# Kernel optimization log

Hardware: AMD Instinct MI355X
Metric: run time of the kernel (lower is better)

Reference implementation:

```python
import jax, jax.numpy as jnp
import numpy as np

LN_EPS = 1e-5


def setup_inputs() -> dict:
    key = jax.random.key(0)
    ks = jax.random.split(key, 8)
    B, N, M, D = 4, 512, 512, 256
    s = 1.0 / np.sqrt(D)
    return {
        "x": jax.random.normal(ks[0], (B, N, D), jnp.float32),
        "c": jax.random.normal(ks[1], (B, M, D), jnp.float32),
        "mask": jnp.ones((B, N, M), jnp.float32),
        "Wq": jax.random.normal(ks[2], (D, D), jnp.float32) * s,
        "bq": jax.random.normal(ks[3], (D,), jnp.float32) * s,
        "Wk": jax.random.normal(ks[4], (D, D), jnp.float32) * s,
        "Wr": jax.random.normal(ks[5], (D,), jnp.float32) * s,
        "Wv": jax.random.normal(ks[6], (D, D), jnp.float32) * s,
        "bv": jax.random.normal(ks[7], (D,), jnp.float32) * s,
        "gamma": jnp.ones((D,), jnp.float32),
        "beta": jnp.zeros((D,), jnp.float32),
    }


def reference(x, c, mask, Wq, bq, Wk, Wr, Wv, bv, gamma, beta):
    D = x.shape[-1]
    deflator = 1.0 / jnp.sqrt(jnp.asarray(D, x.dtype))
    # q: (B, n, 1, d), k: (B, 1, m, d) -- Bahdanau-style additive scores
    q = jnp.tanh(jnp.einsum("bnd,ed->bne", x, Wq) + bq)[:, :, None, :]
    k = jnp.tanh(jnp.einsum("bmd,ed->bme", c, Wk))[:, None, :, :]
    # weight_reduce to scalar score, tanh then relu, squeeze last dim
    w = jax.nn.relu(jnp.tanh(jnp.einsum("bnmd,d->bnm", q + k, Wr)))
    w = w * mask
    v = (jnp.einsum("bmd,ed->bme", c, Wv) + bv) * deflator
    add = jnp.einsum("bnm,bmd->bnd", w, v)
    h = x + add
    mu = jnp.mean(h, axis=-1, keepdims=True)
    var = jnp.mean(jnp.square(h - mu), axis=-1, keepdims=True)
    return (h - mu) / jnp.sqrt(var + LN_EPS) * gamma + beta
```

## Files before the change

### kernel.cpp

```cpp
#include <hip/hip_runtime.h>
#include <math.h>

#define BB 4
#define NN 512
#define MM 512
#define DD 256

typedef short  s16x8  __attribute__((ext_vector_type(8)));
typedef __bf16 bf16x8 __attribute__((ext_vector_type(8)));
typedef __bf16 bf16x4 __attribute__((ext_vector_type(4)));
typedef float  f32x4  __attribute__((ext_vector_type(4)));
typedef float  f32x8  __attribute__((ext_vector_type(8)));
typedef unsigned short u16x4 __attribute__((ext_vector_type(4)));

static __device__ __forceinline__ f32x4 mfma16(s16x8 a, s16x8 b, f32x4 c) {
    return __builtin_amdgcn_mfma_f32_16x16x32_bf16(
        __builtin_bit_cast(bf16x8, a), __builtin_bit_cast(bf16x8, b), c, 0, 0, 0);
}

static __device__ __forceinline__ s16x8 cvt8(const float* __restrict__ p) {
    const float4 a = *(const float4*)p;
    const float4 b = *(const float4*)(p + 4);
    f32x8 f;
    f[0] = a.x; f[1] = a.y; f[2] = a.z; f[3] = a.w;
    f[4] = b.x; f[5] = b.y; f[6] = b.z; f[7] = b.w;
    return __builtin_bit_cast(s16x8, __builtin_convertvector(f, bf16x8));
}

static __device__ __forceinline__ u16x4 cvt4(float x, float y, float z, float w) {
    f32x4 f; f[0] = x; f[1] = y; f[2] = z; f[3] = w;
    return __builtin_bit_cast(u16x4, __builtin_convertvector(f, bf16x4));
}

static __device__ __forceinline__ float tanh_fast(float x) {
    const float e = __builtin_amdgcn_exp2f(x * 2.8853900817779268f);
    return fmaf(-2.0f, __builtin_amdgcn_rcpf(e + 1.0f), 1.0f);
}

__global__ __launch_bounds__(256) void k_proj(
    const float* __restrict__ x, const float* __restrict__ c,
    const float* __restrict__ Wq, const float* __restrict__ bq,
    const float* __restrict__ Wk, const float* __restrict__ Wr,
    const float* __restrict__ Wv, const float* __restrict__ bv,
    float* __restrict__ qs, float* __restrict__ ks,
    unsigned short* __restrict__ vT)
{
    __shared__ float red[4][16];
    const int tid  = threadIdx.x;
    const int lane = tid & 63, w = tid >> 6;
    const int li   = lane & 15, g = lane >> 4;
    const bool isk = blockIdx.x >= 128;
    const int row0 = (blockIdx.x & 127) << 4;
    const float* __restrict__ src = isk ? c : x;

    const float* ap = src + (size_t)(row0 + li) * DD + g * 8;
    s16x8 af[8];
    #pragma unroll
    for (int kk = 0; kk < 8; ++kk) af[kk] = cvt8(ap + kk * 32);

    const int e_base = w * 64 + li;

    if (!isk) {
        f32x4 acc[4];
        const float* bp[4];
        #pragma unroll
        for (int nt = 0; nt < 4; ++nt) {
            acc[nt] = (f32x4){0.f, 0.f, 0.f, 0.f};
            bp[nt] = Wq + (size_t)(e_base + nt * 16) * DD + g * 8;
        }
        #pragma unroll
        for (int kk = 0; kk < 8; ++kk)
            #pragma unroll
            for (int nt = 0; nt < 4; ++nt)
                acc[nt] = mfma16(af[kk], cvt8(bp[nt] + kk * 32), acc[nt]);

        float p[4] = {0.f, 0.f, 0.f, 0.f};
        #pragma unroll
        for (int nt = 0; nt < 4; ++nt) {
            const int e = e_base + nt * 16;
            const float bqe = bq[e], wre = Wr[e];
            #pragma unroll
            for (int r = 0; r < 4; ++r)
                p[r] += wre * tanh_fast(acc[nt][r] + bqe);
        }
        #pragma unroll
        for (int r = 0; r < 4; ++r) {
            p[r] += __shfl_xor(p[r], 1);
            p[r] += __shfl_xor(p[r], 2);
            p[r] += __shfl_xor(p[r], 4);
            p[r] += __shfl_xor(p[r], 8);
        }
        if (li == 0) {
            #pragma unroll
            for (int r = 0; r < 4; ++r) red[w][g * 4 + r] = p[r];
        }
        __syncthreads();
        if (tid < 16)
            qs[row0 + tid] = red[0][tid] + red[1][tid] + red[2][tid] + red[3][tid];
    } else {
        f32x4 ak[4], av[4];
        const float* bpk[4];
        const float* bpv[4];
        #pragma unroll
        for (int nt = 0; nt < 4; ++nt) {
            ak[nt] = (f32x4){0.f, 0.f, 0.f, 0.f};
            av[nt] = (f32x4){0.f, 0.f, 0.f, 0.f};
            bpk[nt] = Wk + (size_t)(e_base + nt * 16) * DD + g * 8;
            bpv[nt] = Wv + (size_t)(e_base + nt * 16) * DD + g * 8;
        }
        #pragma unroll
        for (int kk = 0; kk < 8; ++kk)
            #pragma unroll
            for (int nt = 0; nt < 4; ++nt) {
                ak[nt] = mfma16(af[kk], cvt8(bpk[nt] + kk * 32), ak[nt]);
                av[nt] = mfma16(af[kk], cvt8(bpv[nt] + kk * 32), av[nt]);
            }

        const int b  = row0 >> 9;
        const int m0 = row0 & 511;
        unsigned short* vTb = vT + (size_t)b * (DD * MM);
        #pragma unroll
        for (int nt = 0; nt < 4; ++nt) {
            const int e = e_base + nt * 16;
            const float bve = bv[e];
            const u16x4 o = cvt4((av[nt][0] + bve) * 0.0625f,
                                 (av[nt][1] + bve) * 0.0625f,
                                 (av[nt][2] + bve) * 0.0625f,
                                 (av[nt][3] + bve) * 0.0625f);
            *(u16x4*)(vTb + (size_t)e * MM + m0 + g * 4) = o;
        }

        float p[4] = {0.f, 0.f, 0.f, 0.f};
        #pragma unroll
        for (int nt = 0; nt < 4; ++nt) {
            const int e = e_base + nt * 16;
            const float wre = Wr[e];
            #pragma unroll
            for (int r = 0; r < 4; ++r)
                p[r] += wre * tanh_fast(ak[nt][r]);
        }
        #pragma unroll
        for (int r = 0; r < 4; ++r) {
            p[r] += __shfl_xor(p[r], 1);
            p[r] += __shfl_xor(p[r], 2);
            p[r] += __shfl_xor(p[r], 4);
            p[r] += __shfl_xor(p[r], 8);
        }
        if (li == 0) {
            #pragma unroll
            for (int r = 0; r < 4; ++r) red[w][g * 4 + r] = p[r];
        }
        __syncthreads();
        if (tid < 16)
            ks[row0 + tid] = red[0][tid] + red[1][tid] + red[2][tid] + red[3][tid];
    }
}

__global__ __launch_bounds__(256) void k_main(
    const float* __restrict__ x, const float* __restrict__ mask,
    const float* __restrict__ qs, const float* __restrict__ ks,
    const unsigned short* __restrict__ vT,
    const float* __restrict__ gamma, const float* __restrict__ beta,
    float* __restrict__ out)
{
    __shared__ unsigned short w_lds[16][512];
    __shared__ float ksm[MM];
    __shared__ float h_lds[16][264];
    const int tid  = threadIdx.x;
    const int lane = tid & 63, w = tid >> 6;
    const int li   = lane & 15, g = lane >> 4;
    const int n0g  = blockIdx.x << 3;
    const int b    = n0g >> 9;

    ksm[tid]       = ks[(b << 9) + tid];
    ksm[tid + 256] = ks[(b << 9) + 256 + tid];
    __syncthreads();

    char* wbase = (char*)w_lds;
    const float* __restrict__ mrow = mask + (size_t)n0g * MM;
    #pragma unroll
    for (int it = 0; it < 4; ++it) {
        const int L = (it << 10) + (tid << 2);
        const int i = L >> 9;
        const int m = L & 511;
        const float qv = qs[n0g + i];
        const float4 mk = *(const float4*)(mrow + (size_t)i * MM + m);
        const float4 kv = *(const float4*)&ksm[m];
        const u16x4 o = cvt4(fmaxf(tanh_fast(qv + kv.x), 0.f) * mk.x,
                             fmaxf(tanh_fast(qv + kv.y), 0.f) * mk.y,
                             fmaxf(tanh_fast(qv + kv.z), 0.f) * mk.z,
                             fmaxf(tanh_fast(qv + kv.w), 0.f) * mk.w);
        *(u16x4*)(wbase + (i << 10) + ((m << 1) ^ ((i & 7) << 4))) = o;
    }
    __syncthreads();

    f32x4 acc[4];
    const unsigned short* vp[4];
    #pragma unroll
    for (int nt = 0; nt < 4; ++nt) {
        acc[nt] = (f32x4){0.f, 0.f, 0.f, 0.f};
        vp[nt] = vT + (size_t)b * (DD * MM)
                    + (size_t)(w * 64 + nt * 16 + li) * MM + g * 8;
    }
    const char* arow = wbase + (li << 10);
    const int aswz = (li & 7) << 4;
    #pragma unroll
    for (int kk = 0; kk < 16; ++kk) {
        const s16x8 a = *(const s16x8*)(arow + (((kk << 6) + (g << 4)) ^ aswz));
        #pragma unroll
        for (int nt = 0; nt < 4; ++nt)
            acc[nt] = mfma16(a, *(const s16x8*)(vp[nt] + kk * 32), acc[nt]);
    }

    #pragma unroll
    for (int nt = 0; nt < 4; ++nt) {
        const int e = w * 64 + nt * 16 + li;
        #pragma unroll
        for (int r = 0; r < 4; ++r)
            h_lds[g * 4 + r][e] = acc[nt][r];
    }
    __syncthreads();

    const float4 gm = ((const float4*)gamma)[lane];
    const float4 bt = ((const float4*)beta)[lane];
    #pragma unroll
    for (int rr = 0; rr < 2; ++rr) {
        const int row = (w << 1) + rr;
        const float4 hv = *(const float4*)&h_lds[row][lane << 2];
        const float4 xv = *(const float4*)(x + ((size_t)(n0g + row)) * DD + (lane << 2));
        float4 h;
        h.x = xv.x + hv.x; h.y = xv.y + hv.y;
        h.z = xv.z + hv.z; h.w = xv.w + hv.w;
        float s  = h.x + h.y + h.z + h.w;
        float s2 = h.x * h.x + h.y * h.y + h.z * h.z + h.w * h.w;
        #pragma unroll
        for (int off = 32; off; off >>= 1) {
            s  += __shfl_xor(s, off);
            s2 += __shfl_xor(s2, off);
        }
        const float mean = s * (1.0f / DD);
        const float var  = s2 * (1.0f / DD) - mean * mean;
        const float inv  = rsqrtf(var + 1e-5f);
        float4 o;
        o.x = (h.x - mean) * inv * gm.x + bt.x;
        o.y = (h.y - mean) * inv * gm.y + bt.y;
        o.z = (h.z - mean) * inv * gm.z + bt.z;
        o.w = (h.w - mean) * inv * gm.w + bt.w;
        *(float4*)(out + ((size_t)(n0g + row)) * DD + (lane << 2)) = o;
    }
}

extern "C" void kernel_launch(void* const* d_in, const int* in_sizes, int n_in,
                              void* d_out, int out_size, void* d_ws, size_t ws_size,
                              hipStream_t stream) {
    const float* x     = (const float*)d_in[0];
    const float* c     = (const float*)d_in[1];
    const float* mask  = (const float*)d_in[2];
    const float* Wq    = (const float*)d_in[3];
    const float* bq    = (const float*)d_in[4];
    const float* Wk    = (const float*)d_in[5];
    const float* Wr    = (const float*)d_in[6];
    const float* Wv    = (const float*)d_in[7];
    const float* bv    = (const float*)d_in[8];
    const float* gamma = (const float*)d_in[9];
    const float* beta  = (const float*)d_in[10];
    float* out = (float*)d_out;

    float* ws = (float*)d_ws;
    float* qs  = ws;
    float* ksb = ws + 2048;
    unsigned short* vT = (unsigned short*)(ws + 4096);

    k_proj<<<256, 256, 0, stream>>>(x, c, Wq, bq, Wk, Wr, Wv, bv, qs, ksb, vT);
    k_main<<<256, 256, 0, stream>>>(x, mask, qs, ksb, vT, gamma, beta, out);
}
```

Before: 36.24 us.

## Balance V projection across q/k blocks and prefetch V fragments early

The projection kernel's V GEMM is split so the x-side blocks compute half of the V columns (loading c as well) and the c-side blocks compute the other half. This evens out work between the two block groups, which before were imbalanced because k blocks did both K and V. The main kernel also issues loads for the first four k-steps of V fragments before the score/LDS phase, hiding global latency behind the tanh computation at the cost of extra registers.

After: 38.42 us. 1.06x slower.

```diff
diff --git a/kernel.cpp b/kernel.cpp
--- a/kernel.cpp
+++ b/kernel.cpp
@@ -51,16 +51,22 @@
     const int li   = lane & 15, g = lane >> 4;
     const bool isk = blockIdx.x >= 128;
     const int row0 = (blockIdx.x & 127) << 4;
-    const float* __restrict__ src = isk ? c : x;
-
-    const float* ap = src + (size_t)(row0 + li) * DD + g * 8;
-    s16x8 af[8];
-    #pragma unroll
-    for (int kk = 0; kk < 8; ++kk) af[kk] = cvt8(ap + kk * 32);
-
+    const int b  = row0 >> 9;
+    const int m0 = row0 & 511;
+    unsigned short* vTb = vT + (size_t)b * (DD * MM);
     const int e_base = w * 64 + li;
+    const int e_v    = (isk ? 128 : 0) + w * 32 + li;
 
     if (!isk) {
+        const float* ap = x + (size_t)(row0 + li) * DD + g * 8;
+        s16x8 af[8];
+        #pragma unroll
+        for (int kk = 0; kk < 8; ++kk) af[kk] = cvt8(ap + kk * 32);
+        const float* apc = c + (size_t)(row0 + li) * DD + g * 8;
+        s16x8 afc[8];
+        #pragma unroll
+        for (int kk = 0; kk < 8; ++kk) afc[kk] = cvt8(apc + kk * 32);
+
         f32x4 acc[4];
         const float* bp[4];
         #pragma unroll
@@ -68,11 +74,33 @@
             acc[nt] = (f32x4){0.f, 0.f, 0.f, 0.f};
             bp[nt] = Wq + (size_t)(e_base + nt * 16) * DD + g * 8;
         }
-        #pragma unroll
-        for (int kk = 0; kk < 8; ++kk)
+        f32x4 avv[2];
+        const float* bpv[2];
+        #pragma unroll
+        for (int nt = 0; nt < 2; ++nt) {
+            avv[nt] = (f32x4){0.f, 0.f, 0.f, 0.f};
+            bpv[nt] = Wv + (size_t)(e_v + nt * 16) * DD + g * 8;
+        }
+        #pragma unroll
+        for (int kk = 0; kk < 8; ++kk) {
             #pragma unroll
             for (int nt = 0; nt < 4; ++nt)
                 acc[nt] = mfma16(af[kk], cvt8(bp[nt] + kk * 32), acc[nt]);
+            #pragma unroll
+            for (int nt = 0; nt < 2; ++nt)
+                avv[nt] = mfma16(afc[kk], cvt8(bpv[nt] + kk * 32), avv[nt]);
+        }
+
+        #pragma unroll
+        for (int nt = 0; nt < 2; ++nt) {
+            const int e = e_v + nt * 16;
+            const float bve = bv[e];
+            const u16x4 o = cvt4((avv[nt][0] + bve) * 0.0625f,
+                                 (avv[nt][1] + bve) * 0.0625f,
+                                 (avv[nt][2] + bve) * 0.0625f,
+                                 (avv[nt][3] + bve) * 0.0625f);
+            *(u16x4*)(vTb + (size_t)e * MM + m0 + g * 4) = o;
+        }
 
         float p[4] = {0.f, 0.f, 0.f, 0.f};
         #pragma unroll
@@ -98,35 +126,43 @@
         if (tid < 16)
             qs[row0 + tid] = red[0][tid] + red[1][tid] + red[2][tid] + red[3][tid];
     } else {
-        f32x4 ak[4], av[4];
-        const float* bpk[4];
-        const float* bpv[4];
-        #pragma unroll
-        for (int nt = 0; nt < 4; ++nt) {
-            ak[nt] = (f32x4){0.f, 0.f, 0.f, 0.f};
-            av[nt] = (f32x4){0.f, 0.f, 0.f, 0.f};
-            bpk[nt] = Wk + (size_t)(e_base + nt * 16) * DD + g * 8;
-            bpv[nt] = Wv + (size_t)(e_base + nt * 16) * DD + g * 8;
-        }
-        #pragma unroll
-        for (int kk = 0; kk < 8; ++kk)
-            #pragma unroll
-            for (int nt = 0; nt < 4; ++nt) {
-                ak[nt] = mfma16(af[kk], cvt8(bpk[nt] + kk * 32), ak[nt]);
-                av[nt] = mfma16(af[kk], cvt8(bpv[nt] + kk * 32), av[nt]);
-            }
-
-        const int b  = row0 >> 9;
-        const int m0 = row0 & 511;
-        unsigned short* vTb = vT + (size_t)b * (DD * MM);
-        #pragma unroll
-        for (int nt = 0; nt < 4; ++nt) {
-            const int e = e_base + nt * 16;
+        const float* ap = c + (size_t)(row0 + li) * DD + g * 8;
+        s16x8 af[8];
+        #pragma unroll
+        for (int kk = 0; kk < 8; ++kk) af[kk] = cvt8(ap + kk * 32);
+
+        f32x4 acc[4];
+        const float* bp[4];
+        #pragma unroll
+        for (int nt = 0; nt < 4; ++nt) {
+            acc[nt] = (f32x4){0.f, 0.f, 0.f, 0.f};
+            bp[nt] = Wk + (size_t)(e_base + nt * 16) * DD + g * 8;
+        }
+        f32x4 avv[2];
+        const float* bpv[2];
+        #pragma unroll
+        for (int nt = 0; nt < 2; ++nt) {
+            avv[nt] = (f32x4){0.f, 0.f, 0.f, 0.f};
+            bpv[nt] = Wv + (size_t)(e_v + nt * 16) * DD + g * 8;
+        }
+        #pragma unroll
+        for (int kk = 0; kk < 8; ++kk) {
+            #pragma unroll
+            for (int nt = 0; nt < 4; ++nt)
+                acc[nt] = mfma16(af[kk], cvt8(bp[nt] + kk * 32), acc[nt]);
+            #pragma unroll
+            for (int nt = 0; nt < 2; ++nt)
+                avv[nt] = mfma16(af[kk], cvt8(bpv[nt] + kk * 32), avv[nt]);
+        }
+
+        #pragma unroll
+        for (int nt = 0; nt < 2; ++nt) {
+            const int e = e_v + nt * 16;
             const float bve = bv[e];
-            const u16x4 o = cvt4((av[nt][0] + bve) * 0.0625f,
-                                 (av[nt][1] + bve) * 0.0625f,
-                                 (av[nt][2] + bve) * 0.0625f,
-                                 (av[nt][3] + bve) * 0.0625f);
+            const u16x4 o = cvt4((avv[nt][0] + bve) * 0.0625f,
+                                 (avv[nt][1] + bve) * 0.0625f,
+                                 (avv[nt][2] + bve) * 0.0625f,
+                                 (avv[nt][3] + bve) * 0.0625f);
             *(u16x4*)(vTb + (size_t)e * MM + m0 + g * 4) = o;
         }
 
@@ -137,7 +173,7 @@
             const float wre = Wr[e];
             #pragma unroll
             for (int r = 0; r < 4; ++r)
-                p[r] += wre * tanh_fast(ak[nt][r]);
+                p[r] += wre * tanh_fast(acc[nt][r]);
         }
         #pragma unroll
         for (int r = 0; r < 4; ++r) {
@@ -172,6 +208,18 @@
     const int n0g  = blockIdx.x << 3;
     const int b    = n0g >> 9;
 
+    const unsigned short* vp[4];
+    #pragma unroll
+    for (int nt = 0; nt < 4; ++nt)
+        vp[nt] = vT + (size_t)b * (DD * MM)
+                    + (size_t)(w * 64 + nt * 16 + li) * MM + g * 8;
+    s16x8 vpre[4][4];
+    #pragma unroll
+    for (int kk = 0; kk < 4; ++kk)
+        #pragma unroll
+        for (int nt = 0; nt < 4; ++nt)
+            vpre[kk][nt] = *(const s16x8*)(vp[nt] + kk * 32);
+
     ksm[tid]       = ks[(b << 9) + tid];
     ksm[tid + 256] = ks[(b << 9) + 256 + tid];
     __syncthreads();
@@ -195,21 +243,19 @@
     __syncthreads();
 
     f32x4 acc[4];
-    const unsigned short* vp[4];
-    #pragma unroll
-    for (int nt = 0; nt < 4; ++nt) {
-        acc[nt] = (f32x4){0.f, 0.f, 0.f, 0.f};
-        vp[nt] = vT + (size_t)b * (DD * MM)
-                    + (size_t)(w * 64 + nt * 16 + li) * MM + g * 8;
-    }
+    #pragma unroll
+    for (int nt = 0; nt < 4; ++nt) acc[nt] = (f32x4){0.f, 0.f, 0.f, 0.f};
     const char* arow = wbase + (li << 10);
     const int aswz = (li & 7) << 4;
     #pragma unroll
     for (int kk = 0; kk < 16; ++kk) {
         const s16x8 a = *(const s16x8*)(arow + (((kk << 6) + (g << 4)) ^ aswz));
         #pragma unroll
-        for (int nt = 0; nt < 4; ++nt)
-            acc[nt] = mfma16(a, *(const s16x8*)(vp[nt] + kk * 32), acc[nt]);
+        for (int nt = 0; nt < 4; ++nt) {
+            const s16x8 bfrag = (kk < 4) ? vpre[kk][nt]
+                                         : *(const s16x8*)(vp[nt] + kk * 32);
+            acc[nt] = mfma16(a, bfrag, acc[nt]);
+        }
     }
 
     #pragma unroll
```
